# Kernel optimization log

Measured on AMD Instinct MI355X. Metric: run time of the kernel, lower is better.

## Reference

```python
import jax, jax.numpy as jnp
import numpy as np

PS = 32
EMBED_DIM = 768
IN_CH = 3
IMG = 1024
NUM_PATCHES = 992  # ini_row = i for H=1024, so need i+32 <= 1024
SPIKE_IDX = np.array([5, 300, 800])
SPIKE_VAL = 1.0e6  # makes val ~= 23.94 < 24 -> nearest size 16 -> subdivided


def _token_layout(iw_np, num_patches, ps, H):
    """Replicates the module's data-dependent patch-size / subpatch-position logic.
    Returns static (rows, cols, sizes) for every output token, in emission order."""
    avg = iw_np.mean()
    val = np.minimum(ps * avg ** 0.05 / iw_np ** 0.05, float(ps))
    choices = np.array([32, 16, 8, 4], dtype=np.float64)  # argmin picks first on tie, like min(list)
    sizes = choices[np.argmin(np.abs(val[:, None] - choices[None, :]), axis=1)].astype(np.int64)
    rows, cols, szs = [], [], []
    for i in range(num_patches):
        ini_col = (i * ps) % H
        ini_row = (i * ps * ps) // H
        s = int(sizes[i])
        if 3 < s < ps:
            ns = ps // s  # num_subpatches; subpatch_size == s
            for j in range(ns):
                rows.append(ini_row + (j * s) // ns)
                cols.append(ini_col + (j * s) % (ns * s))
                szs.append(s)
        else:
            rows.append(ini_row)
            cols.append(ini_col)
            szs.append(ps)
    return np.asarray(rows), np.asarray(cols), np.asarray(szs)


def _embed(x, W, b, rows, cols, szs, ps):
    E, C = W.shape[0], W.shape[1]
    B = x.shape[0]
    T = szs.shape[0]
    out = jnp.zeros((B, T, E), dtype=x.dtype)
    for s in np.unique(szs):
        s = int(s)
        idx = np.nonzero(szs == s)[0]  # static token slots for this size group
        r, c = rows[idx], cols[idx]
        if s == ps:
            Wf = W
        else:
            kd = ps // s  # fold the ps x ps kernel down to s x s, as in the module
            Wf = W.reshape(E, C, kd, kd, s, s).sum(axis=(2, 3))
        ar = np.arange(s)
        # gather [B, C, K, s, s] sub-patches with static advanced indexing
        patches = x[:, :, r[:, None, None] + ar[None, :, None], c[:, None, None] + ar[None, None, :]]
        tok = jnp.einsum('bckhw,echw->bke', patches, Wf) + b  # stride==kernel -> 1 token each
        out = out.at[:, jnp.asarray(idx), :].set(tok)
    return out


def setup_inputs() -> dict:
    key = jax.random.key(0)
    k_x, k_w, k_iw, k_b = jax.random.split(key, 4)
    x = jax.random.normal(k_x, (8, IN_CH, IMG, IMG), dtype=jnp.float32)
    iw = jax.random.uniform(k_iw, (1, NUM_PATCHES), dtype=jnp.float32, minval=0.5, maxval=1.5)
    iw = iw.at[0, SPIKE_IDX].set(SPIKE_VAL)  # 3 high-importance patches -> size-16 subdivision
    W = jax.random.normal(k_w, (EMBED_DIM, IN_CH, PS, PS), dtype=jnp.float32) * 0.02
    b = jax.random.normal(k_b, (EMBED_DIM,), dtype=jnp.float32) * 0.02
    return {"x": x, "importance_weights": iw, "W": W, "b": b, "num_patches": NUM_PATCHES}


def reference(x, importance_weights, W, b, num_patches):
    iw = np.asarray(importance_weights)[0]
    rows, cols, szs = _token_layout(iw, int(num_patches), PS, x.shape[3])
    return _embed(x, W, b, rows, cols, szs, PS)  # [B, T, E]
```

## Files before the change

kernel.cpp:

```cpp
#include <hip/hip_runtime.h>


typedef __attribute__((ext_vector_type(8))) short bf16x8;
typedef __attribute__((ext_vector_type(4))) float f32x4;

#define K_DIM 3072
#define N_DIM 768

__device__ __forceinline__ unsigned short f2bf(float f) {
  unsigned int u = __float_as_uint(f);
  u += 0x7fffu + ((u >> 16) & 1u);
  return (unsigned short)(u >> 16);
}

__device__ __forceinline__ void gload16(const void* g, void* l) {
  __builtin_amdgcn_global_load_lds(
      (const __attribute__((address_space(1))) void*)g,
      (__attribute__((address_space(3))) void*)l, 16, 0, 0);
}

__global__ void layout_kernel(const float* __restrict__ iw, int P,
                              int* __restrict__ tokBase, int* __restrict__ tokMask) {
  __shared__ double s_wsum[16];
  __shared__ double s_avg;
  __shared__ int s_cnt[1024];
  int tid = threadIdx.x;
  float v = (tid < P) ? iw[tid] : 0.0f;
  double d = (double)v;
#pragma unroll
  for (int off = 32; off > 0; off >>= 1) d += __shfl_down(d, off, 64);
  if ((tid & 63) == 0) s_wsum[tid >> 6] = d;
  __syncthreads();
  if (tid == 0) {
    double s = 0.0;
    for (int i = 0; i < 16; ++i) s += s_wsum[i];
    s_avg = s / (double)P;
  }
  __syncthreads();
  int cnt = 0, sz = 32;
  if (tid < P) {
    double val = 32.0 * pow(s_avg / (double)v, 0.05);
    if (val > 32.0) val = 32.0;
    sz = (val >= 24.0) ? 32 : (val >= 12.0) ? 16 : (val >= 6.0) ? 8 : 4;
    cnt = (sz < 32) ? (32 / sz) : 1;
  }
  s_cnt[tid] = cnt;
  __syncthreads();
  for (int dl = 1; dl < 1024; dl <<= 1) {
    int add = (tid >= dl) ? s_cnt[tid - dl] : 0;
    __syncthreads();
    s_cnt[tid] += add;
    __syncthreads();
  }
  if (tid < P) {
    int off = s_cnt[tid] - cnt;
    int ini_col = (tid * 32) & 1023;
    int ini_row = (tid * 32 * 32) >> 10;
    if (sz == 32) {
      tokBase[off] = ini_row * 1024 + ini_col;
      tokMask[off] = 31;
    } else {
      int ns = 32 / sz;
      for (int j = 0; j < ns; ++j) {
        int r = ini_row + (j * sz) / ns;
        int c = ini_col + ((j * sz) & 31);
        tokBase[off + j] = r * 1024 + c;
        tokMask[off + j] = sz - 1;
      }
    }
  }
}

__global__ void wconv_kernel(const float* __restrict__ W, unsigned short* __restrict__ Wb,
                             int total4) {
  int idx = blockIdx.x * blockDim.x + threadIdx.x;
  if (idx >= total4) return;
  float4 f = *(const float4*)(W + (size_t)idx * 4);
  ushort4 o;
  o.x = f2bf(f.x); o.y = f2bf(f.y); o.z = f2bf(f.z); o.w = f2bf(f.w);
  *(ushort4*)(Wb + (size_t)idx * 4) = o;
}

__global__ void gather_kernel(const float* __restrict__ x,
                              const int* __restrict__ tokBase,
                              const int* __restrict__ tokMask,
                              unsigned short* __restrict__ Ab,
                              int T, int Mtot, int total4) {
  int idx = blockIdx.x * blockDim.x + threadIdx.x;
  if (idx >= total4) return;
  int m = idx / 768;
  int p = (idx - m * 768) * 4;
  ushort4 o;
  if (m < Mtot) {
    int b = m / T;
    int t = m - b * T;
    int base = tokBase[t];
    int mask = tokMask[t];
    int sh = __popc(mask);
    int c = p >> 10;
    int f = p & 1023;
    int h = (f >> sh) & mask;
    int w = f & mask;
    const float* src = x + (size_t)b * 3145728 + (size_t)c * 1048576 +
                       (size_t)base + (size_t)(h * 1024) + (size_t)w;
    float4 fv = *(const float4*)src;
    o.x = f2bf(fv.x); o.y = f2bf(fv.y); o.z = f2bf(fv.z); o.w = f2bf(fv.w);
  } else {
    o = make_ushort4(0, 0, 0, 0);
  }
  *(ushort4*)(Ab + (size_t)m * K_DIM + p) = o;
}

__global__ __launch_bounds__(256, 2)
void gemm_kernel(const unsigned short* __restrict__ A, const unsigned short* __restrict__ Wb,
                 const float* __restrict__ bias, float* __restrict__ out, int Mtot) {
  __shared__ unsigned short Alds[128 * 32];
  __shared__ unsigned short Blds[128 * 32];
  int tid = threadIdx.x;
  int lane = tid & 63;
  int wave = tid >> 6;
  int wr = wave >> 1, wc = wave & 1;
  int mBase = blockIdx.y * 128;
  int nBase = blockIdx.x * 128;

  f32x4 acc[4][4] = {};

  int sr = lane >> 2;
  int sc = lane & 3;
  const unsigned short* Ag0 = A + (size_t)(mBase + wave * 32 + sr) * K_DIM + sc * 8;
  const unsigned short* Ag1 = Ag0 + (size_t)16 * K_DIM;
  const unsigned short* Bg0 = Wb + (size_t)(nBase + wave * 32 + sr) * K_DIM + sc * 8;
  const unsigned short* Bg1 = Bg0 + (size_t)16 * K_DIM;
  unsigned short* Al0 = Alds + wave * 1024 + lane * 8;
  unsigned short* Al1 = Al0 + 512;
  unsigned short* Bl0 = Blds + wave * 1024 + lane * 8;
  unsigned short* Bl1 = Bl0 + 512;

  int rr = lane & 15, q = lane >> 4;

  for (int k0 = 0; k0 < K_DIM; k0 += 32) {
    gload16(Ag0 + k0, Al0);
    gload16(Ag1 + k0, Al1);
    gload16(Bg0 + k0, Bl0);
    gload16(Bg1 + k0, Bl1);
    __syncthreads();

    bf16x8 aF[4], bF[4];
#pragma unroll
    for (int i = 0; i < 4; ++i)
      aF[i] = *(const bf16x8*)&Alds[(wr * 64 + i * 16 + rr) * 32 + q * 8];
#pragma unroll
    for (int j = 0; j < 4; ++j)
      bF[j] = *(const bf16x8*)&Blds[(wc * 64 + j * 16 + rr) * 32 + q * 8];
#pragma unroll
    for (int i = 0; i < 4; ++i)
#pragma unroll
      for (int j = 0; j < 4; ++j)
        acc[i][j] = __builtin_amdgcn_mfma_f32_16x16x32_bf16(aF[i], bF[j], acc[i][j], 0, 0, 0);
    __syncthreads();
  }

#pragma unroll
  for (int j = 0; j < 4; ++j) {
    int n = nBase + wc * 64 + j * 16 + rr;
    float bv = bias[n];
#pragma unroll
    for (int i = 0; i < 4; ++i) {
      int mrow = mBase + wr * 64 + i * 16 + q * 4;
#pragma unroll
      for (int r2 = 0; r2 < 4; ++r2) {
        int m = mrow + r2;
        if (m < Mtot) out[(size_t)m * N_DIM + n] = acc[i][j][r2] + bv;
      }
    }
  }
}

extern "C" void kernel_launch(void* const* d_in, const int* in_sizes, int n_in,
                              void* d_out, int out_size, void* d_ws, size_t ws_size,
                              hipStream_t stream) {
  const float* x  = (const float*)d_in[0];
  const float* iw = (const float*)d_in[1];
  const float* W  = (const float*)d_in[2];
  const float* b  = (const float*)d_in[3];
  int P = in_sizes[1];
  int B = in_sizes[0] / (3 * 1024 * 1024);
  int E = in_sizes[3];
  int T = out_size / (B * E);
  int Mtot = B * T;
  int Mpad = (Mtot + 127) & ~127;

  char* ws = (char*)d_ws;
  int* tokBase = (int*)ws;
  int* tokMask = (int*)(ws + 32768);
  unsigned short* Wb = (unsigned short*)(ws + 65536);
  unsigned short* Ab = (unsigned short*)(ws + 65536 + (size_t)E * K_DIM * 2);

  layout_kernel<<<1, 1024, 0, stream>>>(iw, P, tokBase, tokMask);

  int w4 = E * K_DIM / 4;
  wconv_kernel<<<(w4 + 255) / 256, 256, 0, stream>>>(W, Wb, w4);

  int a4 = Mpad * (K_DIM / 4);
  gather_kernel<<<(a4 + 255) / 256, 256, 0, stream>>>(x, tokBase, tokMask, Ab, T, Mtot, a4);

  dim3 grid(N_DIM / 128, Mpad / 128);
  gemm_kernel<<<grid, 256, 0, stream>>>(Ab, Wb, b, (float*)d_out, Mtot);
}
```

Baseline: 251.7 us.

## Split-K GEMM with atomic accumulation, fuse prep kernels, per-token gather blocks

The K dimension of the GEMM is split in two along a new grid z axis. The partial results are combined with atomicAdd into an output that is pre-initialized with the bias, which doubles the number of workgroups for the roughly 378-block grid and raises the launch-bounds occupancy hint. Weight conversion, bias broadcast and token layout computation are fused into one multi-role prep kernel to remove launches. The gather now uses one block per (token, batch) and no longer zero-fills padded rows. The costs are extra output traffic from the bias init, fp32 atomics that make summation order nondeterministic, and uninitialized padding rows whose results are masked out.

```diff
diff --git a/kernel.cpp b/kernel.cpp
--- a/kernel.cpp
+++ b/kernel.cpp
@@ -6,6 +6,7 @@
 
 #define K_DIM 3072
 #define N_DIM 768
+#define KSPLIT 2
 
 __device__ __forceinline__ unsigned short f2bf(float f) {
   unsigned int u = __float_as_uint(f);
@@ -19,12 +20,35 @@
       (__attribute__((address_space(3))) void*)l, 16, 0, 0);
 }
 
-__global__ void layout_kernel(const float* __restrict__ iw, int P,
-                              int* __restrict__ tokBase, int* __restrict__ tokMask) {
+__global__ __launch_bounds__(1024)
+void prep_kernel(const float* __restrict__ W, unsigned short* __restrict__ Wb, int w4,
+                 const float* __restrict__ bias, float* __restrict__ out, int out4,
+                 const float* __restrict__ iw, int P,
+                 int* __restrict__ tokBase, int* __restrict__ tokMask,
+                 int NB_W, int NB_BIAS) {
+  int bid = blockIdx.x;
+  int tid = threadIdx.x;
+  if (bid < NB_W) {
+    int idx = bid * 1024 + tid;
+    if (idx < w4) {
+      float4 f = *(const float4*)(W + (size_t)idx * 4);
+      ushort4 o;
+      o.x = f2bf(f.x); o.y = f2bf(f.y); o.z = f2bf(f.z); o.w = f2bf(f.w);
+      *(ushort4*)(Wb + (size_t)idx * 4) = o;
+    }
+    return;
+  }
+  if (bid < NB_W + NB_BIAS) {
+    int idx = (bid - NB_W) * 1024 + tid;
+    if (idx < out4) {
+      int n = (idx % (N_DIM / 4)) * 4;
+      *(float4*)(out + (size_t)idx * 4) = *(const float4*)(bias + n);
+    }
+    return;
+  }
   __shared__ double s_wsum[16];
   __shared__ double s_avg;
   __shared__ int s_cnt[1024];
-  int tid = threadIdx.x;
   float v = (tid < P) ? iw[tid] : 0.0f;
   double d = (double)v;
 #pragma unroll
@@ -71,49 +95,38 @@
   }
 }
 
-__global__ void wconv_kernel(const float* __restrict__ W, unsigned short* __restrict__ Wb,
-                             int total4) {
-  int idx = blockIdx.x * blockDim.x + threadIdx.x;
-  if (idx >= total4) return;
-  float4 f = *(const float4*)(W + (size_t)idx * 4);
-  ushort4 o;
-  o.x = f2bf(f.x); o.y = f2bf(f.y); o.z = f2bf(f.z); o.w = f2bf(f.w);
-  *(ushort4*)(Wb + (size_t)idx * 4) = o;
-}
-
-__global__ void gather_kernel(const float* __restrict__ x,
-                              const int* __restrict__ tokBase,
-                              const int* __restrict__ tokMask,
-                              unsigned short* __restrict__ Ab,
-                              int T, int Mtot, int total4) {
-  int idx = blockIdx.x * blockDim.x + threadIdx.x;
-  if (idx >= total4) return;
-  int m = idx / 768;
-  int p = (idx - m * 768) * 4;
-  ushort4 o;
-  if (m < Mtot) {
-    int b = m / T;
-    int t = m - b * T;
-    int base = tokBase[t];
-    int mask = tokMask[t];
-    int sh = __popc(mask);
+__global__ __launch_bounds__(256)
+void gather_kernel(const float* __restrict__ x,
+                   const int* __restrict__ tokBase,
+                   const int* __restrict__ tokMask,
+                   unsigned short* __restrict__ Ab) {
+  int t = blockIdx.x;
+  int b = blockIdx.y;
+  int T = gridDim.x;
+  int m = b * T + t;
+  int base = tokBase[t];
+  int mask = tokMask[t];
+  int sh = __popc(mask);
+  const float* xb = x + (size_t)b * 3145728 + (size_t)base;
+  unsigned short* arow = Ab + (size_t)m * K_DIM;
+#pragma unroll
+  for (int it = 0; it < 3; ++it) {
+    int g = it * 256 + threadIdx.x;
+    int p = g * 4;
     int c = p >> 10;
     int f = p & 1023;
     int h = (f >> sh) & mask;
     int w = f & mask;
-    const float* src = x + (size_t)b * 3145728 + (size_t)c * 1048576 +
-                       (size_t)base + (size_t)(h * 1024) + (size_t)w;
-    float4 fv = *(const float4*)src;
+    float4 fv = *(const float4*)(xb + (size_t)c * 1048576 + h * 1024 + w);
+    ushort4 o;
     o.x = f2bf(fv.x); o.y = f2bf(fv.y); o.z = f2bf(fv.z); o.w = f2bf(fv.w);
-  } else {
-    o = make_ushort4(0, 0, 0, 0);
-  }
-  *(ushort4*)(Ab + (size_t)m * K_DIM + p) = o;
-}
-
-__global__ __launch_bounds__(256, 2)
+    *(ushort4*)(arow + p) = o;
+  }
+}
+
+__global__ __launch_bounds__(256, 4)
 void gemm_kernel(const unsigned short* __restrict__ A, const unsigned short* __restrict__ Wb,
-                 const float* __restrict__ bias, float* __restrict__ out, int Mtot) {
+                 float* __restrict__ out, int Mtot) {
   __shared__ unsigned short Alds[128 * 32];
   __shared__ unsigned short Blds[128 * 32];
   int tid = threadIdx.x;
@@ -122,14 +135,15 @@
   int wr = wave >> 1, wc = wave & 1;
   int mBase = blockIdx.y * 128;
   int nBase = blockIdx.x * 128;
+  int kBase = blockIdx.z * (K_DIM / KSPLIT);
 
   f32x4 acc[4][4] = {};
 
   int sr = lane >> 2;
   int sc = lane & 3;
-  const unsigned short* Ag0 = A + (size_t)(mBase + wave * 32 + sr) * K_DIM + sc * 8;
+  const unsigned short* Ag0 = A + (size_t)(mBase + wave * 32 + sr) * K_DIM + sc * 8 + kBase;
   const unsigned short* Ag1 = Ag0 + (size_t)16 * K_DIM;
-  const unsigned short* Bg0 = Wb + (size_t)(nBase + wave * 32 + sr) * K_DIM + sc * 8;
+  const unsigned short* Bg0 = Wb + (size_t)(nBase + wave * 32 + sr) * K_DIM + sc * 8 + kBase;
   const unsigned short* Bg1 = Bg0 + (size_t)16 * K_DIM;
   unsigned short* Al0 = Alds + wave * 1024 + lane * 8;
   unsigned short* Al1 = Al0 + 512;
@@ -138,7 +152,7 @@
 
   int rr = lane & 15, q = lane >> 4;
 
-  for (int k0 = 0; k0 < K_DIM; k0 += 32) {
+  for (int k0 = 0; k0 < K_DIM / KSPLIT; k0 += 32) {
     gload16(Ag0 + k0, Al0);
     gload16(Ag1 + k0, Al1);
     gload16(Bg0 + k0, Bl0);
@@ -163,14 +177,13 @@
 #pragma unroll
   for (int j = 0; j < 4; ++j) {
     int n = nBase + wc * 64 + j * 16 + rr;
-    float bv = bias[n];
 #pragma unroll
     for (int i = 0; i < 4; ++i) {
       int mrow = mBase + wr * 64 + i * 16 + q * 4;
 #pragma unroll
       for (int r2 = 0; r2 < 4; ++r2) {
         int m = mrow + r2;
-        if (m < Mtot) out[(size_t)m * N_DIM + n] = acc[i][j][r2] + bv;
+        if (m < Mtot) atomicAdd(&out[(size_t)m * N_DIM + n], acc[i][j][r2]);
       }
     }
   }
@@ -196,14 +209,16 @@
   unsigned short* Wb = (unsigned short*)(ws + 65536);
   unsigned short* Ab = (unsigned short*)(ws + 65536 + (size_t)E * K_DIM * 2);
 
-  layout_kernel<<<1, 1024, 0, stream>>>(iw, P, tokBase, tokMask);
-
   int w4 = E * K_DIM / 4;
-  wconv_kernel<<<(w4 + 255) / 256, 256, 0, stream>>>(W, Wb, w4);
-
-  int a4 = Mpad * (K_DIM / 4);
-  gather_kernel<<<(a4 + 255) / 256, 256, 0, stream>>>(x, tokBase, tokMask, Ab, T, Mtot, a4);
-
-  dim3 grid(N_DIM / 128, Mpad / 128);
-  gemm_kernel<<<grid, 256, 0, stream>>>(Ab, Wb, b, (float*)d_out, Mtot);
-}
+  int out4 = out_size / 4;
+  int NB_W = (w4 + 1023) / 1024;
+  int NB_BIAS = (out4 + 1023) / 1024;
+  prep_kernel<<<NB_W + NB_BIAS + 1, 1024, 0, stream>>>(
+      W, Wb, w4, b, (float*)d_out, out4, iw, P, tokBase, tokMask, NB_W, NB_BIAS);
+
+  dim3 gGrid(T, B);
+  gather_kernel<<<gGrid, 256, 0, stream>>>(x, tokBase, tokMask, Ab);
+
+  dim3 grid(N_DIM / 128, Mpad / 128, KSPLIT);
+  gemm_kernel<<<grid, 256, 0, stream>>>(Ab, Wb, (float*)d_out, Mtot);
+}
```

Measured after the change: 262.9 us. 1.04x slower.

## Pre-swizzle A/B into MFMA fragment layout and drop LDS from GEMM

Applied to the files above, without the earlier changes.

The weight conversion and the patch gather now write bf16 operands directly in a per-16-row, per-32-K fragment-tiled layout that matches the MFMA operand order. This lets the GEMM run as single-wave 64x64 tiles that load fragments straight from global memory into registers, double-buffered, with no LDS staging or barriers. The layout computation and weight conversion are merged into one launch to save a kernel. The trade-off is less data reuse across waves, since each wave refetches its own A/B tiles through cache, and more blocks with smaller tiles.

```diff
diff --git a/kernel.cpp b/kernel.cpp
--- a/kernel.cpp
+++ b/kernel.cpp
@@ -2,6 +2,7 @@
 
 
 typedef __attribute__((ext_vector_type(8))) short bf16x8;
+typedef __attribute__((ext_vector_type(8))) unsigned short u16x8;
 typedef __attribute__((ext_vector_type(4))) float f32x4;
 
 #define K_DIM 3072
@@ -13,18 +14,37 @@
   return (unsigned short)(u >> 16);
 }
 
-__device__ __forceinline__ void gload16(const void* g, void* l) {
-  __builtin_amdgcn_global_load_lds(
-      (const __attribute__((address_space(1))) void*)g,
-      (__attribute__((address_space(3))) void*)l, 16, 0, 0);
-}
-
-__global__ void layout_kernel(const float* __restrict__ iw, int P,
-                              int* __restrict__ tokBase, int* __restrict__ tokMask) {
+__global__ __launch_bounds__(1024)
+void prep_kernel(const float* __restrict__ W, unsigned short* __restrict__ Bf,
+                 const float* __restrict__ iw, int P,
+                 int* __restrict__ tokBase, int* __restrict__ tokMask, int NB_W) {
+  int bid = blockIdx.x;
+  int tid = threadIdx.x;
+  if (bid < NB_W) {
+#pragma unroll
+    for (int s = 0; s < 2; ++s) {
+      int c = bid * 2048 + tid + s * 1024;
+      if (c < 48 * 96 * 64) {
+        int l = c & 63;
+        int u = c >> 6;
+        int g = u % 96;
+        int nt = u / 96;
+        int n = nt * 16 + (l & 15);
+        int k = g * 32 + (l >> 4) * 8;
+        const float* src = W + (size_t)n * K_DIM + k;
+        float4 f0 = *(const float4*)src;
+        float4 f1 = *(const float4*)(src + 4);
+        u16x8 o;
+        o[0] = f2bf(f0.x); o[1] = f2bf(f0.y); o[2] = f2bf(f0.z); o[3] = f2bf(f0.w);
+        o[4] = f2bf(f1.x); o[5] = f2bf(f1.y); o[6] = f2bf(f1.z); o[7] = f2bf(f1.w);
+        *(u16x8*)(Bf + (size_t)c * 8) = o;
+      }
+    }
+    return;
+  }
   __shared__ double s_wsum[16];
   __shared__ double s_avg;
   __shared__ int s_cnt[1024];
-  int tid = threadIdx.x;
   float v = (tid < P) ? iw[tid] : 0.0f;
   double d = (double)v;
 #pragma unroll
@@ -71,102 +91,114 @@
   }
 }
 
-__global__ void wconv_kernel(const float* __restrict__ W, unsigned short* __restrict__ Wb,
-                             int total4) {
-  int idx = blockIdx.x * blockDim.x + threadIdx.x;
-  if (idx >= total4) return;
-  float4 f = *(const float4*)(W + (size_t)idx * 4);
-  ushort4 o;
-  o.x = f2bf(f.x); o.y = f2bf(f.y); o.z = f2bf(f.z); o.w = f2bf(f.w);
-  *(ushort4*)(Wb + (size_t)idx * 4) = o;
-}
-
-__global__ void gather_kernel(const float* __restrict__ x,
-                              const int* __restrict__ tokBase,
-                              const int* __restrict__ tokMask,
-                              unsigned short* __restrict__ Ab,
-                              int T, int Mtot, int total4) {
-  int idx = blockIdx.x * blockDim.x + threadIdx.x;
-  if (idx >= total4) return;
-  int m = idx / 768;
-  int p = (idx - m * 768) * 4;
-  ushort4 o;
-  if (m < Mtot) {
-    int b = m / T;
+__global__ __launch_bounds__(256)
+void gather_kernel(const float* __restrict__ x,
+                   const int* __restrict__ tokBase,
+                   const int* __restrict__ tokMask,
+                   unsigned short* __restrict__ Af, int T, int Mtot) {
+  int mt = blockIdx.x;
+  int tid = threadIdx.x;
+  int l = tid & 63;
+  int g0 = tid >> 6;
+  int m = mt * 16 + (l & 15);
+  int q = l >> 4;
+  bool valid = (m < Mtot);
+  int b = 0, base = 0, mask = 31, sh = 5;
+  if (valid) {
+    b = m / T;
     int t = m - b * T;
-    int base = tokBase[t];
-    int mask = tokMask[t];
-    int sh = __popc(mask);
-    int c = p >> 10;
-    int f = p & 1023;
-    int h = (f >> sh) & mask;
-    int w = f & mask;
-    const float* src = x + (size_t)b * 3145728 + (size_t)c * 1048576 +
-                       (size_t)base + (size_t)(h * 1024) + (size_t)w;
-    float4 fv = *(const float4*)src;
-    o.x = f2bf(fv.x); o.y = f2bf(fv.y); o.z = f2bf(fv.z); o.w = f2bf(fv.w);
-  } else {
-    o = make_ushort4(0, 0, 0, 0);
-  }
-  *(ushort4*)(Ab + (size_t)m * K_DIM + p) = o;
-}
-
-__global__ __launch_bounds__(256, 2)
-void gemm_kernel(const unsigned short* __restrict__ A, const unsigned short* __restrict__ Wb,
+    base = tokBase[t];
+    mask = tokMask[t];
+    sh = __popc(mask);
+  }
+  const float* xb = x + (size_t)b * 3145728 + base;
+  unsigned short* outp = Af + ((size_t)mt * 96 + g0) * 512 + l * 8;
+#pragma unroll
+  for (int i = 0; i < 24; ++i) {
+    int g = g0 + i * 4;
+    int k = g * 32 + q * 8;
+    u16x8 o = {0, 0, 0, 0, 0, 0, 0, 0};
+    if (valid) {
+      int c = k >> 10;
+      int f = k & 1023;
+      if (sh >= 3) {
+        int h = (f >> sh) & mask;
+        int w = f & mask;
+        const float* s = xb + (size_t)c * 1048576 + h * 1024 + w;
+        float4 f0 = *(const float4*)s;
+        float4 f1 = *(const float4*)(s + 4);
+        o[0] = f2bf(f0.x); o[1] = f2bf(f0.y); o[2] = f2bf(f0.z); o[3] = f2bf(f0.w);
+        o[4] = f2bf(f1.x); o[5] = f2bf(f1.y); o[6] = f2bf(f1.z); o[7] = f2bf(f1.w);
+      } else {
+#pragma unroll
+        for (int j = 0; j < 8; ++j) {
+          int ff = f + j;
+          int h = (ff >> sh) & mask;
+          int w = ff & mask;
+          o[j] = f2bf(xb[(size_t)c * 1048576 + h * 1024 + w]);
+        }
+      }
+    }
+    *(u16x8*)(outp + (size_t)i * 2048) = o;
+  }
+}
+
+__global__ __launch_bounds__(64)
+void gemm_kernel(const short* __restrict__ Af, const short* __restrict__ Bf,
                  const float* __restrict__ bias, float* __restrict__ out, int Mtot) {
-  __shared__ unsigned short Alds[128 * 32];
-  __shared__ unsigned short Blds[128 * 32];
-  int tid = threadIdx.x;
-  int lane = tid & 63;
-  int wave = tid >> 6;
-  int wr = wave >> 1, wc = wave & 1;
-  int mBase = blockIdx.y * 128;
-  int nBase = blockIdx.x * 128;
+  int l = threadIdx.x;
+  int wn = blockIdx.x;
+  int wm = blockIdx.y;
+  int loff = l * 8;
+
+  const short* pA[4];
+  const short* pB[4];
+#pragma unroll
+  for (int i = 0; i < 4; ++i) pA[i] = Af + ((size_t)(wm * 4 + i) * 96) * 512 + loff;
+#pragma unroll
+  for (int j = 0; j < 4; ++j) pB[j] = Bf + ((size_t)(wn * 4 + j) * 96) * 512 + loff;
 
   f32x4 acc[4][4] = {};
-
-  int sr = lane >> 2;
-  int sc = lane & 3;
-  const unsigned short* Ag0 = A + (size_t)(mBase + wave * 32 + sr) * K_DIM + sc * 8;
-  const unsigned short* Ag1 = Ag0 + (size_t)16 * K_DIM;
-  const unsigned short* Bg0 = Wb + (size_t)(nBase + wave * 32 + sr) * K_DIM + sc * 8;
-  const unsigned short* Bg1 = Bg0 + (size_t)16 * K_DIM;
-  unsigned short* Al0 = Alds + wave * 1024 + lane * 8;
-  unsigned short* Al1 = Al0 + 512;
-  unsigned short* Bl0 = Blds + wave * 1024 + lane * 8;
-  unsigned short* Bl1 = Bl0 + 512;
-
-  int rr = lane & 15, q = lane >> 4;
-
-  for (int k0 = 0; k0 < K_DIM; k0 += 32) {
-    gload16(Ag0 + k0, Al0);
-    gload16(Ag1 + k0, Al1);
-    gload16(Bg0 + k0, Bl0);
-    gload16(Bg1 + k0, Bl1);
-    __syncthreads();
-
-    bf16x8 aF[4], bF[4];
-#pragma unroll
-    for (int i = 0; i < 4; ++i)
-      aF[i] = *(const bf16x8*)&Alds[(wr * 64 + i * 16 + rr) * 32 + q * 8];
-#pragma unroll
-    for (int j = 0; j < 4; ++j)
-      bF[j] = *(const bf16x8*)&Blds[(wc * 64 + j * 16 + rr) * 32 + q * 8];
-#pragma unroll
-    for (int i = 0; i < 4; ++i)
-#pragma unroll
-      for (int j = 0; j < 4; ++j)
-        acc[i][j] = __builtin_amdgcn_mfma_f32_16x16x32_bf16(aF[i], bF[j], acc[i][j], 0, 0, 0);
-    __syncthreads();
-  }
-
+  bf16x8 a0[4], b0[4], a1[4], b1[4];
+
+#define LOADSET(A_, B_, G_)                                   \
+  {                                                           \
+    _Pragma("unroll")                                         \
+    for (int i = 0; i < 4; ++i)                               \
+      A_[i] = *(const bf16x8*)(pA[i] + (size_t)(G_) * 512);   \
+    _Pragma("unroll")                                         \
+    for (int j = 0; j < 4; ++j)                               \
+      B_[j] = *(const bf16x8*)(pB[j] + (size_t)(G_) * 512);   \
+  }
+#define MFMASET(A_, B_)                                                      \
+  {                                                                          \
+    _Pragma("unroll")                                                        \
+    for (int i = 0; i < 4; ++i)                                              \
+      _Pragma("unroll")                                                      \
+      for (int j = 0; j < 4; ++j)                                            \
+        acc[i][j] = __builtin_amdgcn_mfma_f32_16x16x32_bf16(A_[i], B_[j],    \
+                                                            acc[i][j], 0, 0, 0); \
+  }
+
+  LOADSET(a0, b0, 0);
+  for (int g = 0; g < 94; g += 2) {
+    LOADSET(a1, b1, g + 1);
+    MFMASET(a0, b0);
+    LOADSET(a0, b0, g + 2);
+    MFMASET(a1, b1);
+  }
+  LOADSET(a1, b1, 95);
+  MFMASET(a0, b0);
+  MFMASET(a1, b1);
+
+  int rr = l & 15, q = l >> 4;
 #pragma unroll
   for (int j = 0; j < 4; ++j) {
-    int n = nBase + wc * 64 + j * 16 + rr;
+    int n = wn * 64 + j * 16 + rr;
     float bv = bias[n];
 #pragma unroll
     for (int i = 0; i < 4; ++i) {
-      int mrow = mBase + wr * 64 + i * 16 + q * 4;
+      int mrow = wm * 64 + i * 16 + q * 4;
 #pragma unroll
       for (int r2 = 0; r2 < 4; ++r2) {
         int m = mrow + r2;
@@ -174,6 +206,8 @@
       }
     }
   }
+#undef LOADSET
+#undef MFMASET
 }
 
 extern "C" void kernel_launch(void* const* d_in, const int* in_sizes, int n_in,
@@ -188,22 +222,21 @@
   int E = in_sizes[3];
   int T = out_size / (B * E);
   int Mtot = B * T;
-  int Mpad = (Mtot + 127) & ~127;
+  int Mpad = (Mtot + 63) & ~63;
+  int mtBlocks = Mpad / 16;
 
   char* ws = (char*)d_ws;
   int* tokBase = (int*)ws;
   int* tokMask = (int*)(ws + 32768);
-  unsigned short* Wb = (unsigned short*)(ws + 65536);
-  unsigned short* Ab = (unsigned short*)(ws + 65536 + (size_t)E * K_DIM * 2);
-
-  layout_kernel<<<1, 1024, 0, stream>>>(iw, P, tokBase, tokMask);
-
-  int w4 = E * K_DIM / 4;
-  wconv_kernel<<<(w4 + 255) / 256, 256, 0, stream>>>(W, Wb, w4);
-
-  int a4 = Mpad * (K_DIM / 4);
-  gather_kernel<<<(a4 + 255) / 256, 256, 0, stream>>>(x, tokBase, tokMask, Ab, T, Mtot, a4);
-
-  dim3 grid(N_DIM / 128, Mpad / 128);
-  gemm_kernel<<<grid, 256, 0, stream>>>(Ab, Wb, b, (float*)d_out, Mtot);
-}
+  unsigned short* Bf = (unsigned short*)(ws + 65536);
+  unsigned short* Af = (unsigned short*)(ws + 65536 + (size_t)E * K_DIM * 2);
+
+  int NB_W = (48 * 96 * 64 + 2047) / 2048;
+  prep_kernel<<<NB_W + 1, 1024, 0, stream>>>(W, Bf, iw, P, tokBase, tokMask, NB_W);
+
+  gather_kernel<<<mtBlocks, 256, 0, stream>>>(x, tokBase, tokMask, Af, T, Mtot);
+
+  dim3 grid(N_DIM / 64, Mpad / 64);
+  gemm_kernel<<<grid, 64, 0, stream>>>((const short*)Af, (const short*)Bf, b,
+                                       (float*)d_out, Mtot);
+}
```

After: 249.0 us. Within noise of the previous version (-1.1%).
